# Kernel optimization log

Hardware: AMD Instinct MI355X
Metric: run time of the kernel (lower is better)

## Reference

```python
import jax, jax.numpy as jnp
import numpy as np

INPUT_DIM = 1024
HEADS = 16
HEAD_DIM = 64
OUT_DIM = HEADS * HEAD_DIM
B, S = 4, 2048


def _xavier(key, shape):
    fan_in, fan_out = shape
    limit = float(np.sqrt(6.0 / (fan_in + fan_out)))
    return jax.random.uniform(key, shape, jnp.float32, -limit, limit)


def setup_inputs() -> dict:
    key = jax.random.key(0)
    kq, kk, kv, kwq, kwk, kwv = jax.random.split(key, 6)
    return {
        "query": jax.random.normal(kq, (B, S, INPUT_DIM), jnp.float32),
        "key": jax.random.normal(kk, (B, S, INPUT_DIM), jnp.float32),
        "value": jax.random.normal(kv, (B, S, INPUT_DIM), jnp.float32),
        "WQ": _xavier(kwq, (INPUT_DIM, OUT_DIM)),
        "WK": _xavier(kwk, (INPUT_DIM, OUT_DIM)),
        "WV": _xavier(kwv, (INPUT_DIM, OUT_DIM)),
    }


def reference(query, key, value, WQ, WK, WV):
    b, s, _ = query.shape
    # Project and split into heads: [B, H, S, D]
    q = (query @ WQ).reshape(b, s, HEADS, HEAD_DIM).transpose(0, 2, 1, 3)
    k = (key @ WK).reshape(b, s, HEADS, HEAD_DIM).transpose(0, 2, 1, 3)
    v = (value @ WV).reshape(b, s, HEADS, HEAD_DIM).transpose(0, 2, 1, 3)
    scores = jnp.einsum("bhqd,bhkd->bhqk", q, k) / jnp.sqrt(
        jnp.asarray(HEAD_DIM, q.dtype)
    )
    attn = jax.nn.softmax(scores, axis=-1)
    out = jnp.einsum("bhqk,bhkd->bhqd", attn, v)
    return out.transpose(0, 2, 1, 3).reshape(b, s, OUT_DIM)
```

## Files before the change

### kernel.cpp

```cpp
#include <hip/hip_runtime.h>
#include <stdint.h>

#define HEADS 16
#define HDIM  64
#define NDIM  1024
#define BATCH 4
#define SEQ   2048
#define MTOT  (BATCH * SEQ)

typedef __attribute__((ext_vector_type(8))) short short8;
typedef __attribute__((ext_vector_type(4))) float float4v;
typedef __attribute__((ext_vector_type(4))) int int4v;
typedef __attribute__((ext_vector_type(2))) int int2v;
typedef __attribute__((ext_vector_type(4))) unsigned short ushort4v;

static __device__ __forceinline__ unsigned int fbits(float f) {
    union { float f; unsigned int u; } v; v.f = f; return v.u;
}
static __device__ __forceinline__ unsigned short bf16r(float f) {
    return (unsigned short)((fbits(f) + 0x8000u) >> 16);
}
static __device__ __forceinline__ unsigned int pack2(float lo, float hi) {
    return ((fbits(hi) + 0x8000u) & 0xffff0000u) | ((fbits(lo) + 0x8000u) >> 16);
}
static __device__ __forceinline__ unsigned int cvt_pk_bf16(float lo, float hi) {
    unsigned int r;
    asm("v_cvt_pk_bf16_f32 %0, %1, %2" : "=v"(r) : "v"(lo), "v"(hi));
    return r;
}

static __device__ __forceinline__ void gl_lds16(const unsigned short* g, unsigned short* l) {
    __builtin_amdgcn_global_load_lds(
        (const __attribute__((address_space(1))) unsigned int*)(uintptr_t)g,
        (__attribute__((address_space(3))) unsigned int*)(uintptr_t)l,
        16, 0, 0);
}

__global__ __launch_bounds__(256) void cast_x(
    const float* __restrict__ X0, const float* __restrict__ X1, const float* __restrict__ X2,
    unsigned short* __restrict__ Y0, unsigned short* __restrict__ Y1, unsigned short* __restrict__ Y2)
{
    int z = blockIdx.z;
    const float* X = (z == 0) ? X0 : (z == 1) ? X1 : X2;
    unsigned short* Y = (z == 0) ? Y0 : (z == 1) ? Y1 : Y2;
    size_t i = ((size_t)blockIdx.x * 256 + threadIdx.x) * 8;
    float4v a = *(const float4v*)(X + i);
    float4v b = *(const float4v*)(X + i + 4);
    int4v p;
    p.x = pack2(a.x, a.y); p.y = pack2(a.z, a.w);
    p.z = pack2(b.x, b.y); p.w = pack2(b.z, b.w);
    *(int4v*)(Y + i) = p;
}

__global__ __launch_bounds__(256) void cast_transpose_w(
    const float* __restrict__ W0, const float* __restrict__ W1, const float* __restrict__ W2,
    unsigned short* __restrict__ T0, unsigned short* __restrict__ T1, unsigned short* __restrict__ T2)
{
    const float* W = (blockIdx.z == 0) ? W0 : (blockIdx.z == 1) ? W1 : W2;
    unsigned short* T = (blockIdx.z == 0) ? T0 : (blockIdx.z == 1) ? T1 : T2;
    __shared__ __align__(16) unsigned short tile[64][65];
    int t = threadIdx.x;
    int k0 = blockIdx.y * 64, n0 = blockIdx.x * 64;
    int row = t >> 2, seg = (t & 3) * 16;
    const float* src = W + (size_t)(k0 + row) * NDIM + n0 + seg;
#pragma unroll
    for (int i = 0; i < 4; ++i) {
        float4v v = *(const float4v*)(src + i * 4);
        tile[row][seg + i*4 + 0] = bf16r(v.x);
        tile[row][seg + i*4 + 1] = bf16r(v.y);
        tile[row][seg + i*4 + 2] = bf16r(v.z);
        tile[row][seg + i*4 + 3] = bf16r(v.w);
    }
    __syncthreads();
    unsigned short* dst = T + (size_t)(n0 + row) * NDIM + k0 + seg;
#pragma unroll
    for (int i = 0; i < 4; ++i) {
        ushort4v o;
        o.x = tile[seg + i*4 + 0][row];
        o.y = tile[seg + i*4 + 1][row];
        o.z = tile[seg + i*4 + 2][row];
        o.w = tile[seg + i*4 + 3][row];
        *(ushort4v*)(dst + i*4) = o;
    }
}

#define BM 128
#define BN 128
#define BK 32

__global__ __launch_bounds__(256) void proj_gemm(
    const unsigned short* __restrict__ Xqc, const unsigned short* __restrict__ Xkc,
    const unsigned short* __restrict__ Xvc, const float* __restrict__ Xv32,
    const unsigned short* __restrict__ Tq, const unsigned short* __restrict__ Tk, const unsigned short* __restrict__ Tv,
    unsigned short* __restrict__ Oq, unsigned short* __restrict__ Ok, unsigned short* __restrict__ Ov,
    float qscale, int vasync)
{
    int z = blockIdx.z;
    const unsigned short* Xc = (z == 0) ? Xqc : (z == 1) ? Xkc : Xvc;
    const unsigned short* Wt = (z == 0) ? Tq : (z == 1) ? Tk : Tv;
    unsigned short* Out = (z == 0) ? Oq : (z == 1) ? Ok : Ov;
    float scale = (z == 0) ? qscale : 1.0f;
    bool vtrans = (z == 2);
    bool afast = (z < 2) || (vasync != 0);

    __shared__ __align__(16) unsigned short Asm[BM * BK];
    __shared__ __align__(16) unsigned short Bsm[BN * BK];

    int t = threadIdx.x;
    int wave = t >> 6, lane = t & 63, l15 = lane & 15, quad = lane >> 4;
    int m0 = blockIdx.x * BM, n0 = blockIdx.y * BN;
    int wm = (wave >> 1) * 64, wn = (wave & 1) * 64;

    float4v acc[4][4];
#pragma unroll
    for (int i = 0; i < 4; ++i)
#pragma unroll
        for (int j = 0; j < 4; ++j) acc[i][j] = (float4v){0.f, 0.f, 0.f, 0.f};

    int c0 = t, c1 = t + 256;
    const unsigned short* ga0 = Xc + (size_t)(m0 + (c0 >> 2)) * NDIM + (c0 & 3) * 8;
    const unsigned short* ga1 = Xc + (size_t)(m0 + (c1 >> 2)) * NDIM + (c1 & 3) * 8;
    const float* fa0 = Xv32 + (size_t)(m0 + (c0 >> 2)) * NDIM + (c0 & 3) * 8;
    const float* fa1 = Xv32 + (size_t)(m0 + (c1 >> 2)) * NDIM + (c1 & 3) * 8;
    const unsigned short* gb0 = Wt + (size_t)(n0 + (c0 >> 2)) * NDIM + (c0 & 3) * 8;
    const unsigned short* gb1 = Wt + (size_t)(n0 + (c1 >> 2)) * NDIM + (c1 & 3) * 8;
    unsigned short* as0 = &Asm[c0 * 8];
    unsigned short* as1 = &Asm[c1 * 8];
    unsigned short* bs0 = &Bsm[c0 * 8];
    unsigned short* bs1 = &Bsm[c1 * 8];

    for (int kt = 0; kt < NDIM; kt += BK) {
        __syncthreads();
        if (afast) {
            gl_lds16(ga0 + kt, as0);
            gl_lds16(ga1 + kt, as1);
        } else {
            float4v x0 = *(const float4v*)(fa0 + kt);
            float4v x1 = *(const float4v*)(fa0 + kt + 4);
            float4v y0 = *(const float4v*)(fa1 + kt);
            float4v y1 = *(const float4v*)(fa1 + kt + 4);
            int4v pa0, pa1;
            pa0.x = pack2(x0.x, x0.y); pa0.y = pack2(x0.z, x0.w);
            pa0.z = pack2(x1.x, x1.y); pa0.w = pack2(x1.z, x1.w);
            pa1.x = pack2(y0.x, y0.y); pa1.y = pack2(y0.z, y0.w);
            pa1.z = pack2(y1.x, y1.y); pa1.w = pack2(y1.z, y1.w);
            *(int4v*)as0 = pa0;
            *(int4v*)as1 = pa1;
        }
        gl_lds16(gb0 + kt, bs0);
        gl_lds16(gb1 + kt, bs1);
        __syncthreads();

        short8 af[4], bfr[4];
#pragma unroll
        for (int mt = 0; mt < 4; ++mt)
            af[mt] = *(const short8*)&Asm[(wm + mt * 16 + l15) * BK + quad * 8];
#pragma unroll
        for (int nt = 0; nt < 4; ++nt)
            bfr[nt] = *(const short8*)&Bsm[(wn + nt * 16 + l15) * BK + quad * 8];
#pragma unroll
        for (int mt = 0; mt < 4; ++mt)
#pragma unroll
            for (int nt = 0; nt < 4; ++nt)
                acc[mt][nt] = __builtin_amdgcn_mfma_f32_16x16x32_bf16(af[mt], bfr[nt], acc[mt][nt], 0, 0, 0);
    }

#pragma unroll
    for (int mt = 0; mt < 4; ++mt) {
        int mbase = m0 + wm + mt * 16 + quad * 4;
        int b = mbase >> 11;
        int s = mbase & 2047;
#pragma unroll
        for (int nt = 0; nt < 4; ++nt) {
            int gn = n0 + wn + nt * 16 + l15;
            int h = gn >> 6, d = gn & 63;
            if (!vtrans) {
                size_t base = ((size_t)((b * HEADS + h) * SEQ + s)) * HDIM + d;
#pragma unroll
                for (int r = 0; r < 4; ++r)
                    Out[base + (size_t)r * HDIM] = bf16r(acc[mt][nt][r] * scale);
            } else {
                size_t base = ((size_t)((b * HEADS + h) * HDIM + d)) * SEQ + s;
                ushort4v o;
                o.x = bf16r(acc[mt][nt][0]);
                o.y = bf16r(acc[mt][nt][1]);
                o.z = bf16r(acc[mt][nt][2]);
                o.w = bf16r(acc[mt][nt][3]);
                *(ushort4v*)(Out + base) = o;
            }
        }
    }
}

#define BQ  128
#define BKC 64

__global__ __launch_bounds__(256) void attn_kernel(
    const unsigned short* __restrict__ Q,
    const unsigned short* __restrict__ K,
    const unsigned short* __restrict__ Vt,
    float* __restrict__ Out)
{
    __shared__ __align__(16) unsigned short Ksm[BKC][72];
    __shared__ __align__(16) unsigned short Vsm[HDIM][72];
    __shared__ __align__(16) unsigned short Psm[4][32][72];

    int t = threadIdx.x;
    int wave = t >> 6, lane = t & 63, l15 = lane & 15, quad = lane >> 4;
    int L = blockIdx.x;
    int bh = L & 63;
    int b = bh >> 4, h = bh & 15;
    int q0 = (L >> 6) * BQ;

    const unsigned short* Qbh = Q + (size_t)bh * SEQ * HDIM;
    const unsigned short* Kbh = K + (size_t)bh * SEQ * HDIM;
    const unsigned short* Vbh = Vt + (size_t)bh * HDIM * SEQ;

    short8 qf[2][2];
#pragma unroll
    for (int mt = 0; mt < 2; ++mt) {
        int qr = q0 + wave * 32 + mt * 16 + l15;
        qf[mt][0] = *(const short8*)(Qbh + (size_t)qr * HDIM + quad * 8);
        qf[mt][1] = *(const short8*)(Qbh + (size_t)qr * HDIM + 32 + quad * 8);
    }

    float lsum[2][4];
    float4v acc_o[2][4];
#pragma unroll
    for (int mt = 0; mt < 2; ++mt) {
#pragma unroll
        for (int r = 0; r < 4; ++r) lsum[mt][r] = 0.f;
#pragma unroll
        for (int dtt = 0; dtt < 4; ++dtt) acc_o[mt][dtt] = (float4v){0.f, 0.f, 0.f, 0.f};
    }

    int srow = t >> 2;
    int sseg = (t & 3) * 16;
    const unsigned short* kptr = Kbh + (size_t)srow * HDIM + sseg;
    const unsigned short* vptr = Vbh + (size_t)srow * SEQ + sseg;

    short8 kv0 = *(const short8*)(kptr);
    short8 kv1 = *(const short8*)(kptr + 8);
    short8 kv2 = *(const short8*)(vptr);
    short8 kv3 = *(const short8*)(vptr + 8);

    for (int kc = 0; kc < SEQ; kc += BKC) {
        __syncthreads();
        *(short8*)&Ksm[srow][sseg]     = kv0;
        *(short8*)&Ksm[srow][sseg + 8] = kv1;
        *(short8*)&Vsm[srow][sseg]     = kv2;
        *(short8*)&Vsm[srow][sseg + 8] = kv3;
        __syncthreads();

        int kn = kc + BKC;
        if (kn < SEQ) {
            kv0 = *(const short8*)(kptr + (size_t)kn * HDIM);
            kv1 = *(const short8*)(kptr + (size_t)kn * HDIM + 8);
            kv2 = *(const short8*)(vptr + kn);
            kv3 = *(const short8*)(vptr + kn + 8);
        }

        float4v sc[2][4];
#pragma unroll
        for (int mt = 0; mt < 2; ++mt)
#pragma unroll
            for (int nt = 0; nt < 4; ++nt) sc[mt][nt] = (float4v){0.f, 0.f, 0.f, 0.f};
        __builtin_amdgcn_s_setprio(1);
#pragma unroll
        for (int nt = 0; nt < 4; ++nt) {
            short8 kf0 = *(const short8*)&Ksm[l15 * 4 + nt][quad * 8];
            short8 kf1 = *(const short8*)&Ksm[l15 * 4 + nt][32 + quad * 8];
#pragma unroll
            for (int mt = 0; mt < 2; ++mt) {
                sc[mt][nt] = __builtin_amdgcn_mfma_f32_16x16x32_bf16(qf[mt][0], kf0, sc[mt][nt], 0, 0, 0);
                sc[mt][nt] = __builtin_amdgcn_mfma_f32_16x16x32_bf16(qf[mt][1], kf1, sc[mt][nt], 0, 0, 0);
            }
        }
        __builtin_amdgcn_s_setprio(0);

#pragma unroll
        for (int mt = 0; mt < 2; ++mt)
#pragma unroll
            for (int r = 0; r < 4; ++r) {
                float p0 = __builtin_amdgcn_exp2f(sc[mt][0][r]);
                float p1 = __builtin_amdgcn_exp2f(sc[mt][1][r]);
                float p2 = __builtin_amdgcn_exp2f(sc[mt][2][r]);
                float p3 = __builtin_amdgcn_exp2f(sc[mt][3][r]);
                lsum[mt][r] += (p0 + p1) + (p2 + p3);
                int row = mt * 16 + quad * 4 + r;
                int2v pw;
                pw.x = (int)cvt_pk_bf16(p0, p1);
                pw.y = (int)cvt_pk_bf16(p2, p3);
                *(int2v*)&Psm[wave][row][l15 * 4] = pw;
            }

        __builtin_amdgcn_s_setprio(1);
#pragma unroll
        for (int kseg = 0; kseg < 2; ++kseg) {
            short8 pf0 = *(const short8*)&Psm[wave][l15][kseg * 32 + quad * 8];
            short8 pf1 = *(const short8*)&Psm[wave][16 + l15][kseg * 32 + quad * 8];
#pragma unroll
            for (int dtt = 0; dtt < 4; ++dtt) {
                short8 vf = *(const short8*)&Vsm[dtt * 16 + l15][kseg * 32 + quad * 8];
                acc_o[0][dtt] = __builtin_amdgcn_mfma_f32_16x16x32_bf16(pf0, vf, acc_o[0][dtt], 0, 0, 0);
                acc_o[1][dtt] = __builtin_amdgcn_mfma_f32_16x16x32_bf16(pf1, vf, acc_o[1][dtt], 0, 0, 0);
            }
        }
        __builtin_amdgcn_s_setprio(0);
    }

#pragma unroll
    for (int mt = 0; mt < 2; ++mt)
#pragma unroll
        for (int r = 0; r < 4; ++r) {
            float l = lsum[mt][r];
            l += __shfl_xor(l, 1);
            l += __shfl_xor(l, 2);
            l += __shfl_xor(l, 4);
            l += __shfl_xor(l, 8);
            float inv = 1.0f / l;
            int qrow = q0 + wave * 32 + mt * 16 + quad * 4 + r;
            size_t base = ((size_t)(b * SEQ + qrow)) * NDIM + h * HDIM;
#pragma unroll
            for (int dtt = 0; dtt < 4; ++dtt)
                Out[base + dtt * 16 + l15] = acc_o[mt][dtt][r] * inv;
        }
}

extern "C" void kernel_launch(void* const* d_in, const int* in_sizes, int n_in,
                              void* d_out, int out_size, void* d_ws, size_t ws_size,
                              hipStream_t stream)
{
    const float* q_in = (const float*)d_in[0];
    const float* k_in = (const float*)d_in[1];
    const float* v_in = (const float*)d_in[2];
    const float* WQ = (const float*)d_in[3];
    const float* WK = (const float*)d_in[4];
    const float* WV = (const float*)d_in[5];
    float* out = (float*)d_out;

    unsigned short* ws = (unsigned short*)d_ws;
    size_t wsz = (size_t)NDIM * NDIM;
    size_t psz = (size_t)MTOT * NDIM;
    unsigned short* Tq = ws;
    unsigned short* Tk = Tq + wsz;
    unsigned short* Tv = Tk + wsz;
    unsigned short* Qp = Tv + wsz;
    unsigned short* Kp = Qp + psz;
    unsigned short* Vp = Kp + psz;
    unsigned short* Xvc = Vp + psz;

    unsigned short* Xqc = (unsigned short*)d_out;
    unsigned short* Xkc = Xqc + psz;

    size_t need = (3 * wsz + 4 * psz) * sizeof(unsigned short);
    int vasync = (ws_size >= need) ? 1 : 0;

    cast_x<<<dim3(MTOT * NDIM / (256 * 8), 1, vasync ? 3 : 2), 256, 0, stream>>>(
        q_in, k_in, v_in, Xqc, Xkc, Xvc);
    cast_transpose_w<<<dim3(16, 16, 3), 256, 0, stream>>>(WQ, WK, WV, Tq, Tk, Tv);
    proj_gemm<<<dim3(MTOT / BM, NDIM / BN, 3), 256, 0, stream>>>(
        Xqc, Xkc, Xvc, v_in, Tq, Tk, Tv, Qp, Kp, Vp, 0.125f * 1.44269504088896f, vasync);
    attn_kernel<<<dim3(SEQ / BQ * BATCH * HEADS), 256, 0, stream>>>(Qp, Kp, Vp, out);
}
```

Before: 307.5 us.

## Double query tile per attention block to 64 rows per wave

```diff
diff --git a/kernel.cpp b/kernel.cpp
--- a/kernel.cpp
+++ b/kernel.cpp
@@ -192,7 +192,7 @@
     }
 }
 
-#define BQ  128
+#define BQ  256
 #define BKC 64
 
 __global__ __launch_bounds__(256) void attn_kernel(
@@ -203,7 +203,7 @@
 {
     __shared__ __align__(16) unsigned short Ksm[BKC][72];
     __shared__ __align__(16) unsigned short Vsm[HDIM][72];
-    __shared__ __align__(16) unsigned short Psm[4][32][72];
+    __shared__ __align__(16) unsigned short Psm[4][64][72];
 
     int t = threadIdx.x;
     int wave = t >> 6, lane = t & 63, l15 = lane & 15, quad = lane >> 4;
@@ -216,18 +216,18 @@
     const unsigned short* Kbh = K + (size_t)bh * SEQ * HDIM;
     const unsigned short* Vbh = Vt + (size_t)bh * HDIM * SEQ;
 
-    short8 qf[2][2];
-#pragma unroll
-    for (int mt = 0; mt < 2; ++mt) {
-        int qr = q0 + wave * 32 + mt * 16 + l15;
+    short8 qf[4][2];
+#pragma unroll
+    for (int mt = 0; mt < 4; ++mt) {
+        int qr = q0 + wave * 64 + mt * 16 + l15;
         qf[mt][0] = *(const short8*)(Qbh + (size_t)qr * HDIM + quad * 8);
         qf[mt][1] = *(const short8*)(Qbh + (size_t)qr * HDIM + 32 + quad * 8);
     }
 
-    float lsum[2][4];
-    float4v acc_o[2][4];
-#pragma unroll
-    for (int mt = 0; mt < 2; ++mt) {
+    float lsum[4][4];
+    float4v acc_o[4][4];
+#pragma unroll
+    for (int mt = 0; mt < 4; ++mt) {
 #pragma unroll
         for (int r = 0; r < 4; ++r) lsum[mt][r] = 0.f;
 #pragma unroll
@@ -260,32 +260,32 @@
             kv3 = *(const short8*)(vptr + kn + 8);
         }
 
-        float4v sc[2][4];
-#pragma unroll
-        for (int mt = 0; mt < 2; ++mt)
-#pragma unroll
-            for (int nt = 0; nt < 4; ++nt) sc[mt][nt] = (float4v){0.f, 0.f, 0.f, 0.f};
-        __builtin_amdgcn_s_setprio(1);
+        short8 kf[4][2];
 #pragma unroll
         for (int nt = 0; nt < 4; ++nt) {
-            short8 kf0 = *(const short8*)&Ksm[l15 * 4 + nt][quad * 8];
-            short8 kf1 = *(const short8*)&Ksm[l15 * 4 + nt][32 + quad * 8];
-#pragma unroll
-            for (int mt = 0; mt < 2; ++mt) {
-                sc[mt][nt] = __builtin_amdgcn_mfma_f32_16x16x32_bf16(qf[mt][0], kf0, sc[mt][nt], 0, 0, 0);
-                sc[mt][nt] = __builtin_amdgcn_mfma_f32_16x16x32_bf16(qf[mt][1], kf1, sc[mt][nt], 0, 0, 0);
+            kf[nt][0] = *(const short8*)&Ksm[l15 * 4 + nt][quad * 8];
+            kf[nt][1] = *(const short8*)&Ksm[l15 * 4 + nt][32 + quad * 8];
+        }
+
+#pragma unroll
+        for (int mt = 0; mt < 4; ++mt) {
+            float4v sc[4];
+#pragma unroll
+            for (int nt = 0; nt < 4; ++nt) sc[nt] = (float4v){0.f, 0.f, 0.f, 0.f};
+            __builtin_amdgcn_s_setprio(1);
+#pragma unroll
+            for (int nt = 0; nt < 4; ++nt) {
+                sc[nt] = __builtin_amdgcn_mfma_f32_16x16x32_bf16(qf[mt][0], kf[nt][0], sc[nt], 0, 0, 0);
+                sc[nt] = __builtin_amdgcn_mfma_f32_16x16x32_bf16(qf[mt][1], kf[nt][1], sc[nt], 0, 0, 0);
             }
-        }
-        __builtin_amdgcn_s_setprio(0);
-
-#pragma unroll
-        for (int mt = 0; mt < 2; ++mt)
+            __builtin_amdgcn_s_setprio(0);
+
 #pragma unroll
             for (int r = 0; r < 4; ++r) {
-                float p0 = __builtin_amdgcn_exp2f(sc[mt][0][r]);
-                float p1 = __builtin_amdgcn_exp2f(sc[mt][1][r]);
-                float p2 = __builtin_amdgcn_exp2f(sc[mt][2][r]);
-                float p3 = __builtin_amdgcn_exp2f(sc[mt][3][r]);
+                float p0 = __builtin_amdgcn_exp2f(sc[0][r]);
+                float p1 = __builtin_amdgcn_exp2f(sc[1][r]);
+                float p2 = __builtin_amdgcn_exp2f(sc[2][r]);
+                float p3 = __builtin_amdgcn_exp2f(sc[3][r]);
                 lsum[mt][r] += (p0 + p1) + (p2 + p3);
                 int row = mt * 16 + quad * 4 + r;
                 int2v pw;
@@ -293,24 +293,29 @@
                 pw.y = (int)cvt_pk_bf16(p2, p3);
                 *(int2v*)&Psm[wave][row][l15 * 4] = pw;
             }
+        }
 
         __builtin_amdgcn_s_setprio(1);
 #pragma unroll
         for (int kseg = 0; kseg < 2; ++kseg) {
-            short8 pf0 = *(const short8*)&Psm[wave][l15][kseg * 32 + quad * 8];
-            short8 pf1 = *(const short8*)&Psm[wave][16 + l15][kseg * 32 + quad * 8];
-#pragma unroll
-            for (int dtt = 0; dtt < 4; ++dtt) {
-                short8 vf = *(const short8*)&Vsm[dtt * 16 + l15][kseg * 32 + quad * 8];
-                acc_o[0][dtt] = __builtin_amdgcn_mfma_f32_16x16x32_bf16(pf0, vf, acc_o[0][dtt], 0, 0, 0);
-                acc_o[1][dtt] = __builtin_amdgcn_mfma_f32_16x16x32_bf16(pf1, vf, acc_o[1][dtt], 0, 0, 0);
-            }
+            short8 pf[4], vf[4];
+#pragma unroll
+            for (int mt = 0; mt < 4; ++mt)
+                pf[mt] = *(const short8*)&Psm[wave][mt * 16 + l15][kseg * 32 + quad * 8];
+#pragma unroll
+            for (int dtt = 0; dtt < 4; ++dtt)
+                vf[dtt] = *(const short8*)&Vsm[dtt * 16 + l15][kseg * 32 + quad * 8];
+#pragma unroll
+            for (int mt = 0; mt < 4; ++mt)
+#pragma unroll
+                for (int dtt = 0; dtt < 4; ++dtt)
+                    acc_o[mt][dtt] = __builtin_amdgcn_mfma_f32_16x16x32_bf16(pf[mt], vf[dtt], acc_o[mt][dtt], 0, 0, 0);
         }
         __builtin_amdgcn_s_setprio(0);
     }
 
 #pragma unroll
-    for (int mt = 0; mt < 2; ++mt)
+    for (int mt = 0; mt < 4; ++mt)
 #pragma unroll
         for (int r = 0; r < 4; ++r) {
             float l = lsum[mt][r];
@@ -319,7 +324,7 @@
             l += __shfl_xor(l, 4);
             l += __shfl_xor(l, 8);
             float inv = 1.0f / l;
-            int qrow = q0 + wave * 32 + mt * 16 + quad * 4 + r;
+            int qrow = q0 + wave * 64 + mt * 16 + quad * 4 + r;
             size_t base = ((size_t)(b * SEQ + qrow)) * NDIM + h * HDIM;
 #pragma unroll
             for (int dtt = 0; dtt < 4; ++dtt)
```

New measurement: 308.6 us. Within noise of the previous version (+0.3%).
